# Performance work log

Hardware: AMD Instinct MI355X
Metric: run time of the kernel (lower is better)

Reference implementation:

```python
import jax, jax.numpy as jnp
import numpy as np

B, T, F = 4, 1024, 512
H = 8
DK = F // H
SPAN = 100
PAD_L = int(SPAN * 0.5)          # 50
PAD_R = SPAN - PAD_L - 1         # 49


def setup_inputs() -> dict:
    key = jax.random.key(0)
    ks = jax.random.split(key, 12)
    s = 0.02
    return {
        "query": jax.random.normal(ks[0], (B, T, F), jnp.float32),
        "key": jax.random.normal(ks[1], (B, T, F), jnp.float32),
        "value": jax.random.normal(ks[2], (B, T, F), jnp.float32),
        "mask": jnp.ones((B, 1, T), jnp.int32),
        "Wq": jax.random.normal(ks[3], (F, F), jnp.float32) * s,
        "bq": jnp.zeros((F,), jnp.float32),
        "Wk": jax.random.normal(ks[4], (F, F), jnp.float32) * s,
        "bk": jnp.zeros((F,), jnp.float32),
        "Wv": jax.random.normal(ks[5], (F, F), jnp.float32) * s,
        "bv": jnp.zeros((F,), jnp.float32),
        "Wo": jax.random.normal(ks[6], (F, F), jnp.float32) * s,
        "bo": jnp.zeros((F,), jnp.float32),
    }


def reference(query, key, value, mask, Wq, bq, Wk, bk, Wv, bv, Wo, bo):
    b, t, f = query.shape
    # projections -> (b, h, t, d_k)
    q = (query @ Wq + bq).reshape(b, t, H, DK).transpose(0, 2, 1, 3)
    k = (key @ Wk + bk).reshape(b, t, H, DK).transpose(0, 2, 1, 3)
    v = (value @ Wv + bv).reshape(b, t, H, DK).transpose(0, 2, 1, 3)

    # pad time axis and gather sliding windows: window for query i covers
    # original positions [i - PAD_L, i + PAD_R]
    k_pad = jnp.pad(k, ((0, 0), (0, 0), (PAD_L, PAD_R), (0, 0)))
    v_pad = jnp.pad(v, ((0, 0), (0, 0), (PAD_L, PAD_R), (0, 0)))
    idx = jnp.arange(t)[:, None] + jnp.arange(SPAN)[None, :]   # (t, span)
    new_k = k_pad[:, :, idx, :]   # (b, h, t, span, d_k)
    new_v = v_pad[:, :, idx, :]   # (b, h, t, span, d_k)

    scores = jnp.einsum("bhtd,bhtsd->bhts", q, new_k) / jnp.sqrt(
        jnp.asarray(DK, q.dtype)
    )

    # banded mask: mask is (b, 1, t) key-padding mask, expanded over queries;
    # unfold_mask extracts mask[b, i-PAD_L : i+PAD_R+1] with 0-padding at edges
    m = mask[:, 0, :]                               # (b, t)
    m_pad = jnp.pad(m, ((0, 0), (PAD_L, PAD_R)))    # (b, t + span - 1)
    band = m_pad[:, idx]                            # (b, t, span)
    invalid = (band == 0)[:, None, :, :]            # (b, 1, t, span)

    min_val = jnp.finfo(scores.dtype).min
    scores = jnp.where(invalid, min_val, scores)
    attn = jax.nn.softmax(scores, axis=-1)
    attn = jnp.where(invalid, 0.0, attn)

    x = jnp.einsum("bhts,bhtsd->bhtd", attn, new_v)
    x = x.transpose(0, 2, 1, 3).reshape(b, t, H * DK)
    return x @ Wo + bo
```

## Files before the change

### kernel.cpp

```cpp
#include <hip/hip_runtime.h>
#include <hip/hip_bf16.h>

#define BB 4
#define TT 1024
#define FF 512
#define HH 8
#define DKK 64
#define VROW 1152

typedef unsigned short u16;
typedef u16 u16x8 __attribute__((ext_vector_type(8)));
typedef __bf16 bf16x8 __attribute__((ext_vector_type(8)));
typedef float f32x4 __attribute__((ext_vector_type(4)));

__device__ __forceinline__ u16 f2bf(float f) {
  unsigned u = __builtin_bit_cast(unsigned, f);
  u += 0x7FFFu + ((u >> 16) & 1u);
  return (u16)(u >> 16);
}

__device__ __forceinline__ f32x4 mfma16(u16x8 a, u16x8 b, f32x4 c) {
  return __builtin_amdgcn_mfma_f32_16x16x32_bf16(
      __builtin_bit_cast(bf16x8, a), __builtin_bit_cast(bf16x8, b), c, 0, 0, 0);
}

__device__ __forceinline__ u16x8 ld8(const u16* p) {
  return *reinterpret_cast<const u16x8*>(p);
}

__global__ __launch_bounds__(256) void cvt_x(const float* __restrict__ q,
                                             const float* __restrict__ k,
                                             const float* __restrict__ v,
                                             u16* __restrict__ o) {
  long idx = ((long)blockIdx.x * 256 + threadIdx.x) * 8;
  const long NPER = (long)BB * TT * FF;
  int w = (int)(idx / NPER);
  long lo = idx - (long)w * NPER;
  const float* s = (w == 0) ? q : ((w == 1) ? k : v);
  const float4* sp = reinterpret_cast<const float4*>(s + lo);
  float4 f0 = sp[0], f1 = sp[1];
  u16x8 r;
  r[0] = f2bf(f0.x); r[1] = f2bf(f0.y); r[2] = f2bf(f0.z); r[3] = f2bf(f0.w);
  r[4] = f2bf(f1.x); r[5] = f2bf(f1.y); r[6] = f2bf(f1.z); r[7] = f2bf(f1.w);
  *reinterpret_cast<u16x8*>(o + idx) = r;
}

__global__ void cvt_w(const float* __restrict__ Wq, const float* __restrict__ Wk,
                      const float* __restrict__ Wv, const float* __restrict__ Wo,
                      u16* __restrict__ Wt) {
  __shared__ u16 tile[32][33];
  int w = blockIdx.z;
  const float* W = (w == 0) ? Wq : (w == 1) ? Wk : (w == 2) ? Wv : Wo;
  int n0 = blockIdx.x * 32, k0 = blockIdx.y * 32;
  int tx = threadIdx.x, ty = threadIdx.y;
#pragma unroll
  for (int i = 0; i < 4; i++) {
    int kk = ty + i * 8;
    tile[kk][tx] = f2bf(W[(size_t)(k0 + kk) * FF + n0 + tx]);
  }
  __syncthreads();
#pragma unroll
  for (int i = 0; i < 4; i++) {
    int nn = ty + i * 8;
    Wt[(size_t)w * FF * FF + (size_t)(n0 + nn) * FF + k0 + tx] = tile[tx][nn];
  }
}

__global__ __launch_bounds__(256) void gemm_qkv(
    const u16* __restrict__ Xc, const u16* __restrict__ Wt,
    const float* __restrict__ bq, const float* __restrict__ bk,
    const float* __restrict__ bv,
    u16* __restrict__ Qb, u16* __restrict__ Kb, u16* __restrict__ Vt) {
  int z = blockIdx.z;
  const u16* A = Xc + (size_t)z * BB * TT * FF;
  const u16* Bt = Wt + (size_t)z * FF * FF;
  const float* bias = (z == 0) ? bq : ((z == 1) ? bk : bv);
  int tid = threadIdx.x, wid = tid >> 6, lane = tid & 63;
  int cl = lane & 15, g = lane >> 4;
  int m0 = blockIdx.x * 64 + (wid >> 1) * 32;
  int n0 = blockIdx.y * 64 + (wid & 1) * 32;
  f32x4 acc[2][2] = {};
  const u16* a0p = A + (size_t)(m0 + cl) * FF + g * 8;
  const u16* a1p = a0p + (size_t)16 * FF;
  const u16* b0p = Bt + (size_t)(n0 + cl) * FF + g * 8;
  const u16* b1p = b0p + (size_t)16 * FF;
#pragma unroll 4
  for (int k0 = 0; k0 < FF; k0 += 32) {
    u16x8 a0 = ld8(a0p + k0), a1 = ld8(a1p + k0);
    u16x8 w0 = ld8(b0p + k0), w1 = ld8(b1p + k0);
    acc[0][0] = mfma16(a0, w0, acc[0][0]);
    acc[0][1] = mfma16(a0, w1, acc[0][1]);
    acc[1][0] = mfma16(a1, w0, acc[1][0]);
    acc[1][1] = mfma16(a1, w1, acc[1][1]);
  }
#pragma unroll
  for (int rt = 0; rt < 2; rt++)
#pragma unroll
    for (int ct = 0; ct < 2; ct++)
#pragma unroll
      for (int r = 0; r < 4; r++) {
        int m = m0 + rt * 16 + g * 4 + r;
        int n = n0 + ct * 16 + cl;
        float v = acc[rt][ct][r] + bias[n];
        int b = m >> 10, t = m & 1023, h = n >> 6, d = n & 63;
        size_t bh = (size_t)b * HH + h;
        if (z == 0)
          Qb[(bh * TT + t) * DKK + d] = f2bf(v * 0.125f);
        else if (z == 1)
          Kb[(bh * TT + t) * DKK + d] = f2bf(v);
        else
          Vt[(bh * DKK + d) * VROW + 64 + t] = f2bf(v);
      }
}

__global__ __launch_bounds__(256) void attn(const u16* __restrict__ Qb,
                                            const u16* __restrict__ Kb,
                                            const u16* __restrict__ Vt,
                                            const int* __restrict__ mask,
                                            u16* __restrict__ X2) {
  __shared__ u16 plds[4][16][128];
  int tid = threadIdx.x, wid = tid >> 6, lane = tid & 63;
  int cl = lane & 15, g = lane >> 4;
  int bh = blockIdx.x >> 4;
  int qt = ((blockIdx.x & 15) << 2) + wid;
  int t0 = qt << 4;
  int b = bh >> 3, h = bh & 7;

  const u16* qrow = Qb + ((size_t)bh * TT + t0 + cl) * DKK + g * 8;
  u16x8 qa0 = ld8(qrow);
  u16x8 qa1 = ld8(qrow + 32);

  f32x4 s[8];
#pragma unroll
  for (int c = 0; c < 8; c++) {
    int kt = t0 - 50 + c * 16 + cl;
    bool inr = (kt >= 0) && (kt < TT);
    bool valid = inr && (mask[b * TT + (inr ? kt : 0)] != 0);
    u16x8 kb0 = {0, 0, 0, 0, 0, 0, 0, 0}, kb1 = {0, 0, 0, 0, 0, 0, 0, 0};
    if (inr) {
      const u16* kp = Kb + ((size_t)bh * TT + kt) * DKK + g * 8;
      kb0 = ld8(kp);
      kb1 = ld8(kp + 32);
    }
    f32x4 acc = {0.f, 0.f, 0.f, 0.f};
    acc = mfma16(qa0, kb0, acc);
    acc = mfma16(qa1, kb1, acc);
#pragma unroll
    for (int r = 0; r < 4; r++) {
      int row = g * 4 + r;
      int j = c * 16 + cl;
      int sp = j - row;
      bool ok = valid && (sp >= 0) && (sp < 100);
      acc[r] = ok ? acc[r] : -1e30f;
    }
    s[c] = acc;
  }

#pragma unroll
  for (int r = 0; r < 4; r++) {
    float m = s[0][r];
#pragma unroll
    for (int c = 1; c < 8; c++) m = fmaxf(m, s[c][r]);
    m = fmaxf(m, __shfl_xor(m, 1, 64));
    m = fmaxf(m, __shfl_xor(m, 2, 64));
    m = fmaxf(m, __shfl_xor(m, 4, 64));
    m = fmaxf(m, __shfl_xor(m, 8, 64));
    float sum = 0.f;
#pragma unroll
    for (int c = 0; c < 8; c++) {
      float p = __expf(s[c][r] - m);
      s[c][r] = p;
      sum += p;
    }
    sum += __shfl_xor(sum, 1, 64);
    sum += __shfl_xor(sum, 2, 64);
    sum += __shfl_xor(sum, 4, 64);
    sum += __shfl_xor(sum, 8, 64);
    float inv = 1.0f / sum;
#pragma unroll
    for (int c = 0; c < 8; c++) s[c][r] *= inv;
  }

#pragma unroll
  for (int c = 0; c < 8; c++)
#pragma unroll
    for (int r = 0; r < 4; r++) {
      int row = g * 4 + r;
      int col = (c * 16 + cl) ^ ((row & 7) << 3);
      plds[wid][row][col] = f2bf(s[c][r]);
    }
  __syncthreads();

  u16x8 pa[4];
#pragma unroll
  for (int ks = 0; ks < 4; ks++) {
    int jb = (ks * 32 + g * 8) ^ ((cl & 7) << 3);
    pa[ks] = ld8(&plds[wid][cl][jb]);
  }

  f32x4 o[4] = {};
  const u16* vbase = Vt + (size_t)bh * DKK * VROW;
#pragma unroll
  for (int nt = 0; nt < 4; nt++) {
    int d = nt * 16 + cl;
    const u16* vp = vbase + (size_t)d * VROW + (t0 + 14 + g * 8);
#pragma unroll
    for (int ks = 0; ks < 4; ks++) o[nt] = mfma16(pa[ks], ld8(vp + ks * 32), o[nt]);
  }

#pragma unroll
  for (int nt = 0; nt < 4; nt++)
#pragma unroll
    for (int r = 0; r < 4; r++) {
      int t = t0 + g * 4 + r;
      int f = h * 64 + nt * 16 + cl;
      X2[((size_t)b * TT + t) * FF + f] = f2bf(o[nt][r]);
    }
}

__global__ __launch_bounds__(256) void gemm_out(const u16* __restrict__ X2,
                                                const u16* __restrict__ Wto,
                                                const float* __restrict__ bo,
                                                float* __restrict__ out) {
  int tid = threadIdx.x, wid = tid >> 6, lane = tid & 63;
  int cl = lane & 15, g = lane >> 4;
  int m0 = blockIdx.x * 64 + (wid >> 1) * 32;
  int n0 = blockIdx.y * 64 + (wid & 1) * 32;
  f32x4 acc[2][2] = {};
  const u16* a0p = X2 + (size_t)(m0 + cl) * FF + g * 8;
  const u16* a1p = a0p + (size_t)16 * FF;
  const u16* b0p = Wto + (size_t)(n0 + cl) * FF + g * 8;
  const u16* b1p = b0p + (size_t)16 * FF;
#pragma unroll 4
  for (int k0 = 0; k0 < FF; k0 += 32) {
    u16x8 a0 = ld8(a0p + k0), a1 = ld8(a1p + k0);
    u16x8 w0 = ld8(b0p + k0), w1 = ld8(b1p + k0);
    acc[0][0] = mfma16(a0, w0, acc[0][0]);
    acc[0][1] = mfma16(a0, w1, acc[0][1]);
    acc[1][0] = mfma16(a1, w0, acc[1][0]);
    acc[1][1] = mfma16(a1, w1, acc[1][1]);
  }
#pragma unroll
  for (int rt = 0; rt < 2; rt++)
#pragma unroll
    for (int ct = 0; ct < 2; ct++)
#pragma unroll
      for (int r = 0; r < 4; r++) {
        int m = m0 + rt * 16 + g * 4 + r;
        int n = n0 + ct * 16 + cl;
        out[(size_t)m * FF + n] = acc[rt][ct][r] + bo[n];
      }
}

extern "C" void kernel_launch(void* const* d_in, const int* in_sizes, int n_in,
                              void* d_out, int out_size, void* d_ws, size_t ws_size,
                              hipStream_t stream) {
  const float* query = (const float*)d_in[0];
  const float* key_i = (const float*)d_in[1];
  const float* value = (const float*)d_in[2];
  const int* mask = (const int*)d_in[3];
  const float* Wq = (const float*)d_in[4];
  const float* bq = (const float*)d_in[5];
  const float* Wk = (const float*)d_in[6];
  const float* bk = (const float*)d_in[7];
  const float* Wv = (const float*)d_in[8];
  const float* bv = (const float*)d_in[9];
  const float* Wo = (const float*)d_in[10];
  const float* bo = (const float*)d_in[11];
  float* out = (float*)d_out;

  char* ws = (char*)d_ws;
  u16* Xc = (u16*)(ws + 0);
  u16* Wt = (u16*)(ws + 12582912);
  u16* Qb = (u16*)(ws + 14680064);
  u16* Kb = (u16*)(ws + 18874368);
  u16* Vt = (u16*)(ws + 23068672);
  u16* X2 = (u16*)(ws + 27787264);

  hipLaunchKernelGGL(cvt_x, dim3(3072), dim3(256), 0, stream, query, key_i, value, Xc);
  hipLaunchKernelGGL(cvt_w, dim3(16, 16, 4), dim3(32, 8), 0, stream, Wq, Wk, Wv, Wo, Wt);
  hipLaunchKernelGGL(gemm_qkv, dim3(64, 8, 3), dim3(256), 0, stream,
                     Xc, Wt, bq, bk, bv, Qb, Kb, Vt);
  hipLaunchKernelGGL(attn, dim3(512), dim3(256), 0, stream, Qb, Kb, Vt, mask, X2);
  hipLaunchKernelGGL(gemm_out, dim3(64, 8), dim3(256), 0, stream,
                     X2, Wt + (size_t)3 * FF * FF, bo, out);
}
```

Before: 174.5 us.

## Stage GEMM tiles through LDS with 128x128 blocks and single-wave attention blocks

Rewrites both projection GEMMs to load 128x128 tiles with K-step 32 into shared memory via global_load_lds. Each wave then computes a 64x64 sub-tile from LDS, where before each wave streamed its operands straight from global memory. This raises data reuse and cuts redundant global traffic, but the K-loop is synchronous with no double buffering. The attention kernel is split into 64-thread blocks, one wave each, to give finer scheduling granularity. Since each wave already owned its own LDS slice, this mainly drops the block-wide barrier coupling.

```diff
diff --git a/kernel.cpp b/kernel.cpp
--- a/kernel.cpp
+++ b/kernel.cpp
@@ -7,6 +7,7 @@
 #define HH 8
 #define DKK 64
 #define VROW 1152
+#define BKK 32
 
 typedef unsigned short u16;
 typedef u16 u16x8 __attribute__((ext_vector_type(8)));
@@ -27,6 +28,11 @@
 __device__ __forceinline__ u16x8 ld8(const u16* p) {
   return *reinterpret_cast<const u16x8*>(p);
 }
+
+#define GLDS16(gp, lp)                                              \
+  __builtin_amdgcn_global_load_lds(                                 \
+      (const __attribute__((address_space(1))) void*)(gp),          \
+      (__attribute__((address_space(3))) void*)(lp), 16, 0, 0)
 
 __global__ __launch_bounds__(256) void cvt_x(const float* __restrict__ q,
                                              const float* __restrict__ k,
@@ -66,43 +72,80 @@
   }
 }
 
-__global__ __launch_bounds__(256) void gemm_qkv(
+__device__ __forceinline__ void gemm_tile_core(const u16* __restrict__ A,
+                                               const u16* __restrict__ Bt,
+                                               u16* As, u16* Bs,
+                                               int m_base, int n_base,
+                                               f32x4 (&acc)[4][4]) {
+  int tid = threadIdx.x, wid = tid >> 6, lane = tid & 63;
+  int cl = lane & 15, g = lane >> 4;
+  int wm = (wid >> 1) * 64, wn = (wid & 1) * 64;
+
+  int srow = tid >> 2;
+  int scol = (tid & 3) * 8;
+  const u16* ga0 = A + (size_t)(m_base + srow) * FF + scol;
+  const u16* ga1 = ga0 + (size_t)64 * FF;
+  const u16* gb0 = Bt + (size_t)(n_base + srow) * FF + scol;
+  const u16* gb1 = gb0 + (size_t)64 * FF;
+  u16* la0 = As + wid * 512;
+  u16* la1 = As + 2048 + wid * 512;
+  u16* lb0 = Bs + wid * 512;
+  u16* lb1 = Bs + 2048 + wid * 512;
+
+  const u16* ra = As + (wm + cl) * BKK + g * 8;
+  const u16* rb = Bs + (wn + cl) * BKK + g * 8;
+
+  for (int k0 = 0; k0 < FF; k0 += BKK) {
+    if (k0) __syncthreads();
+    GLDS16(ga0 + k0, la0);
+    GLDS16(ga1 + k0, la1);
+    GLDS16(gb0 + k0, lb0);
+    GLDS16(gb1 + k0, lb1);
+    __syncthreads();
+
+    u16x8 af[4], bf[4];
+#pragma unroll
+    for (int i = 0; i < 4; i++) {
+      af[i] = ld8(ra + i * 16 * BKK);
+      bf[i] = ld8(rb + i * 16 * BKK);
+    }
+#pragma unroll
+    for (int mf = 0; mf < 4; mf++)
+#pragma unroll
+      for (int nf = 0; nf < 4; nf++)
+        acc[mf][nf] = mfma16(af[mf], bf[nf], acc[mf][nf]);
+  }
+}
+
+__global__ __launch_bounds__(256, 3) void gemm_qkv(
     const u16* __restrict__ Xc, const u16* __restrict__ Wt,
     const float* __restrict__ bq, const float* __restrict__ bk,
     const float* __restrict__ bv,
     u16* __restrict__ Qb, u16* __restrict__ Kb, u16* __restrict__ Vt) {
-  int z = blockIdx.z;
-  const u16* A = Xc + (size_t)z * BB * TT * FF;
-  const u16* Bt = Wt + (size_t)z * FF * FF;
+  __shared__ u16 As[128 * BKK];
+  __shared__ u16 Bs[128 * BKK];
+  int m_base = blockIdx.x * 128;
+  int n_base = blockIdx.y * 128;
+  int z = n_base >> 9;
+  const u16* A = Xc + (size_t)z * (BB * TT * FF);
+  f32x4 acc[4][4] = {};
+  gemm_tile_core(A, Wt, As, Bs, m_base, n_base, acc);
+
   const float* bias = (z == 0) ? bq : ((z == 1) ? bk : bv);
   int tid = threadIdx.x, wid = tid >> 6, lane = tid & 63;
   int cl = lane & 15, g = lane >> 4;
-  int m0 = blockIdx.x * 64 + (wid >> 1) * 32;
-  int n0 = blockIdx.y * 64 + (wid & 1) * 32;
-  f32x4 acc[2][2] = {};
-  const u16* a0p = A + (size_t)(m0 + cl) * FF + g * 8;
-  const u16* a1p = a0p + (size_t)16 * FF;
-  const u16* b0p = Bt + (size_t)(n0 + cl) * FF + g * 8;
-  const u16* b1p = b0p + (size_t)16 * FF;
-#pragma unroll 4
-  for (int k0 = 0; k0 < FF; k0 += 32) {
-    u16x8 a0 = ld8(a0p + k0), a1 = ld8(a1p + k0);
-    u16x8 w0 = ld8(b0p + k0), w1 = ld8(b1p + k0);
-    acc[0][0] = mfma16(a0, w0, acc[0][0]);
-    acc[0][1] = mfma16(a0, w1, acc[0][1]);
-    acc[1][0] = mfma16(a1, w0, acc[1][0]);
-    acc[1][1] = mfma16(a1, w1, acc[1][1]);
-  }
-#pragma unroll
-  for (int rt = 0; rt < 2; rt++)
-#pragma unroll
-    for (int ct = 0; ct < 2; ct++)
+  int wm = (wid >> 1) * 64, wn = (wid & 1) * 64;
+  int nb = n_base & 511;
+#pragma unroll
+  for (int mf = 0; mf < 4; mf++)
+#pragma unroll
+    for (int nf = 0; nf < 4; nf++)
 #pragma unroll
       for (int r = 0; r < 4; r++) {
-        int m = m0 + rt * 16 + g * 4 + r;
-        int n = n0 + ct * 16 + cl;
-        float v = acc[rt][ct][r] + bias[n];
-        int b = m >> 10, t = m & 1023, h = n >> 6, d = n & 63;
+        int m = m_base + wm + mf * 16 + g * 4 + r;
+        int nl = nb + wn + nf * 16 + cl;
+        float v = acc[mf][nf][r] + bias[nl];
+        int b = m >> 10, t = m & 1023, h = nl >> 6, d = nl & 63;
         size_t bh = (size_t)b * HH + h;
         if (z == 0)
           Qb[(bh * TT + t) * DKK + d] = f2bf(v * 0.125f);
@@ -113,16 +156,16 @@
       }
 }
 
-__global__ __launch_bounds__(256) void attn(const u16* __restrict__ Qb,
-                                            const u16* __restrict__ Kb,
-                                            const u16* __restrict__ Vt,
-                                            const int* __restrict__ mask,
-                                            u16* __restrict__ X2) {
-  __shared__ u16 plds[4][16][128];
-  int tid = threadIdx.x, wid = tid >> 6, lane = tid & 63;
+__global__ __launch_bounds__(64) void attn(const u16* __restrict__ Qb,
+                                           const u16* __restrict__ Kb,
+                                           const u16* __restrict__ Vt,
+                                           const int* __restrict__ mask,
+                                           u16* __restrict__ X2) {
+  __shared__ u16 plds[16][128];
+  int lane = threadIdx.x & 63;
   int cl = lane & 15, g = lane >> 4;
-  int bh = blockIdx.x >> 4;
-  int qt = ((blockIdx.x & 15) << 2) + wid;
+  int bh = blockIdx.x >> 6;
+  int qt = blockIdx.x & 63;
   int t0 = qt << 4;
   int b = bh >> 3, h = bh & 7;
 
@@ -187,7 +230,7 @@
     for (int r = 0; r < 4; r++) {
       int row = g * 4 + r;
       int col = (c * 16 + cl) ^ ((row & 7) << 3);
-      plds[wid][row][col] = f2bf(s[c][r]);
+      plds[row][col] = f2bf(s[c][r]);
     }
   __syncthreads();
 
@@ -195,7 +238,7 @@
 #pragma unroll
   for (int ks = 0; ks < 4; ks++) {
     int jb = (ks * 32 + g * 8) ^ ((cl & 7) << 3);
-    pa[ks] = ld8(&plds[wid][cl][jb]);
+    pa[ks] = ld8(&plds[cl][jb]);
   }
 
   f32x4 o[4] = {};
@@ -218,37 +261,29 @@
     }
 }
 
-__global__ __launch_bounds__(256) void gemm_out(const u16* __restrict__ X2,
-                                                const u16* __restrict__ Wto,
-                                                const float* __restrict__ bo,
-                                                float* __restrict__ out) {
+__global__ __launch_bounds__(256, 3) void gemm_out(const u16* __restrict__ X2,
+                                                   const u16* __restrict__ Wto,
+                                                   const float* __restrict__ bo,
+                                                   float* __restrict__ out) {
+  __shared__ u16 As[128 * BKK];
+  __shared__ u16 Bs[128 * BKK];
+  int m_base = blockIdx.x * 128;
+  int n_base = blockIdx.y * 128;
+  f32x4 acc[4][4] = {};
+  gemm_tile_core(X2, Wto, As, Bs, m_base, n_base, acc);
+
   int tid = threadIdx.x, wid = tid >> 6, lane = tid & 63;
   int cl = lane & 15, g = lane >> 4;
-  int m0 = blockIdx.x * 64 + (wid >> 1) * 32;
-  int n0 = blockIdx.y * 64 + (wid & 1) * 32;
-  f32x4 acc[2][2] = {};
-  const u16* a0p = X2 + (size_t)(m0 + cl) * FF + g * 8;
-  const u16* a1p = a0p + (size_t)16 * FF;
-  const u16* b0p = Wto + (size_t)(n0 + cl) * FF + g * 8;
-  const u16* b1p = b0p + (size_t)16 * FF;
-#pragma unroll 4
-  for (int k0 = 0; k0 < FF; k0 += 32) {
-    u16x8 a0 = ld8(a0p + k0), a1 = ld8(a1p + k0);
-    u16x8 w0 = ld8(b0p + k0), w1 = ld8(b1p + k0);
-    acc[0][0] = mfma16(a0, w0, acc[0][0]);
-    acc[0][1] = mfma16(a0, w1, acc[0][1]);
-    acc[1][0] = mfma16(a1, w0, acc[1][0]);
-    acc[1][1] = mfma16(a1, w1, acc[1][1]);
-  }
-#pragma unroll
-  for (int rt = 0; rt < 2; rt++)
-#pragma unroll
-    for (int ct = 0; ct < 2; ct++)
+  int wm = (wid >> 1) * 64, wn = (wid & 1) * 64;
+#pragma unroll
+  for (int mf = 0; mf < 4; mf++)
+#pragma unroll
+    for (int nf = 0; nf < 4; nf++)
 #pragma unroll
       for (int r = 0; r < 4; r++) {
-        int m = m0 + rt * 16 + g * 4 + r;
-        int n = n0 + ct * 16 + cl;
-        out[(size_t)m * FF + n] = acc[rt][ct][r] + bo[n];
+        int m = m_base + wm + mf * 16 + g * 4 + r;
+        int n = n_base + wn + nf * 16 + cl;
+        out[(size_t)m * FF + n] = acc[mf][nf][r] + bo[n];
       }
 }
 
@@ -279,9 +314,9 @@
 
   hipLaunchKernelGGL(cvt_x, dim3(3072), dim3(256), 0, stream, query, key_i, value, Xc);
   hipLaunchKernelGGL(cvt_w, dim3(16, 16, 4), dim3(32, 8), 0, stream, Wq, Wk, Wv, Wo, Wt);
-  hipLaunchKernelGGL(gemm_qkv, dim3(64, 8, 3), dim3(256), 0, stream,
+  hipLaunchKernelGGL(gemm_qkv, dim3(32, 12), dim3(256), 0, stream,
                      Xc, Wt, bq, bk, bv, Qb, Kb, Vt);
-  hipLaunchKernelGGL(attn, dim3(512), dim3(256), 0, stream, Qb, Kb, Vt, mask, X2);
-  hipLaunchKernelGGL(gemm_out, dim3(64, 8), dim3(256), 0, stream,
+  hipLaunchKernelGGL(attn, dim3(2048), dim3(64), 0, stream, Qb, Kb, Vt, mask, X2);
+  hipLaunchKernelGGL(gemm_out, dim3(32, 4), dim3(256), 0, stream,
                      X2, Wt + (size_t)3 * FF * FF, bo, out);
 }
```

After: 144.0 us. 17.5% less time.
